# Kernel optimization log

Measured on AMD Instinct MI355X. Metric: run time of the kernel, lower is better.

The kernel has to match this reference:

```python
import jax, jax.numpy as jnp
import numpy as np

NP, P, H, NB = 14, 16, 12, 6  # n_patches per side, patch size, heads, blocks
HD, EMB, SEQ = 64, 768, NP * NP + 1


def _layernorm(x, g, b, eps=1e-5):
    m = x.mean(axis=-1, keepdims=True)
    v = x.var(axis=-1, keepdims=True)
    return (x - m) * jax.lax.rsqrt(v + eps) * g + b


def setup_inputs() -> dict:
    key = jax.random.key(0)
    ks = jax.random.split(key, 16)
    s = 0.02
    B = 64
    inp = {
        "images": jax.random.normal(ks[0], (B, 3, 224, 224), jnp.float32),
        "Wmap": jax.random.normal(ks[1], (768, 768), jnp.float32) * s,
        "bmap": jnp.zeros((768,), jnp.float32),
        "cls_tok": jax.random.normal(ks[2], (1, 768), jnp.float32) * s,
        "pos": jax.random.normal(ks[3], (SEQ, 768), jnp.float32) * s,
        "ln1_g": jnp.ones((NB, 768), jnp.float32),
        "ln1_b": jnp.zeros((NB, 768), jnp.float32),
        "Wq": jax.random.normal(ks[4], (NB, H, HD, HD), jnp.float32) * s,
        "bq": jnp.zeros((NB, H, HD), jnp.float32),
        "Wk": jax.random.normal(ks[5], (NB, H, HD, HD), jnp.float32) * s,
        "bk": jnp.zeros((NB, H, HD), jnp.float32),
        "Wv": jax.random.normal(ks[6], (NB, H, HD, HD), jnp.float32) * s,
        "bv": jnp.zeros((NB, H, HD), jnp.float32),
        "ln2_g": jnp.ones((NB, 768), jnp.float32),
        "ln2_b": jnp.zeros((NB, 768), jnp.float32),
        "W1": jax.random.normal(ks[7], (NB, 768, 3072), jnp.float32) * s,
        "b1": jnp.zeros((NB, 3072), jnp.float32),
        "W2": jax.random.normal(ks[8], (NB, 3072, 768), jnp.float32) * s,
        "b2": jnp.zeros((NB, 768), jnp.float32),
        "Whead": jax.random.normal(ks[9], (768, 10), jnp.float32) * s,
        "bhead": jnp.zeros((10,), jnp.float32),
    }
    return inp


def reference(images, Wmap, bmap, cls_tok, pos, ln1_g, ln1_b, Wq, bq, Wk, bk,
              Wv, bv, ln2_g, ln2_b, W1, b1, W2, b2, Whead, bhead):
    B = images.shape[0]
    # patchify: (B,3,224,224) -> (B,196,768); per-patch channel-first flatten
    x = images.reshape(B, 3, NP, P, NP, P)
    x = x.transpose(0, 2, 4, 1, 3, 5).reshape(B, NP * NP, 3 * P * P)
    tokens = x @ Wmap + bmap  # (B,196,768)
    tokens = jnp.concatenate(
        [jnp.broadcast_to(cls_tok[None], (B, 1, EMB)), tokens], axis=1)
    out = tokens + pos[None]  # (B,197,768)
    scale = 1.0 / jnp.sqrt(jnp.asarray(H, out.dtype))  # NOTE: source divides by sqrt(num_heads)
    for i in range(NB):
        h = _layernorm(out, ln1_g[i], ln1_b[i])
        xh = h.reshape(B, SEQ, H, HD)
        q = jnp.einsum('bshd,hde->bshe', xh, Wq[i]) + bq[i]
        k = jnp.einsum('bshd,hde->bshe', xh, Wk[i]) + bk[i]
        v = jnp.einsum('bshd,hde->bshe', xh, Wv[i]) + bv[i]
        attn = jax.nn.softmax(
            jnp.einsum('bqhd,bkhd->bhqk', q, k) * scale, axis=-1)
        o = jnp.einsum('bhqk,bkhd->bqhd', attn, v).reshape(B, SEQ, EMB)
        out = out + o
        h2 = _layernorm(out, ln2_g[i], ln2_b[i])
        mlp = jax.nn.gelu(h2 @ W1[i] + b1[i], approximate=False) @ W2[i] + b2[i]
        out = out + mlp
    cls = out[:, 0]  # (B,768)
    return jax.nn.softmax(cls @ Whead + bhead, axis=-1)
```

## Files before the change

kernel.cpp:

```cpp
#include <hip/hip_runtime.h>
#include <cstddef>

#define BATCH 64
#define SEQL  197
#define EMB   768
#define NH    12
#define HDIM  64
#define NBLK  6
#define MLPD  3072
#define TOKS  12608
#define PTOK  12544
#define ATT_SCALE 0.28867513459481287f
#define LOG2E 1.4426950408889634f

typedef short bf16x8 __attribute__((ext_vector_type(8)));
typedef float f32x4  __attribute__((ext_vector_type(4)));

__device__ inline float bf2f(unsigned short u) {
  union { unsigned int i; float f; } c; c.i = ((unsigned int)u) << 16; return c.f;
}
__device__ inline unsigned short f2bf(float f) {
  union { float f; unsigned int i; } c; c.f = f;
  unsigned int r = c.i + 0x7FFFu + ((c.i >> 16) & 1u);
  return (unsigned short)(r >> 16);
}

__device__ __forceinline__ void gload16(const unsigned short* g, void* l) {
  __builtin_amdgcn_global_load_lds(
      (const __attribute__((address_space(1))) unsigned int*)g,
      (__attribute__((address_space(3))) unsigned int*)l, 16, 0, 0);
}

__global__ __launch_bounds__(256) void patchify_kernel(const float* __restrict__ img,
                                                       unsigned short* __restrict__ out) {
  int i4 = blockIdx.x * 256 + threadIdx.x;
  int f4 = i4 % 192;
  int r  = i4 / 192;
  int b  = r / 196, t = r - b * 196;
  int f  = f4 * 4;
  int c  = f >> 8;
  int rem = f & 255;
  int iy = rem >> 4, ix = rem & 15;
  int py = t / 14, px = t - py * 14;
  const float* src = img + ((((size_t)b * 3 + c) * 224 + py * 16 + iy) * 224 + px * 16 + ix);
  float4 v = *(const float4*)src;
  ushort4 u;
  u.x = f2bf(v.x); u.y = f2bf(v.y); u.z = f2bf(v.z); u.w = f2bf(v.w);
  *(ushort4*)(out + (size_t)r * 768 + f) = u;
}

__global__ __launch_bounds__(256) void clspos_kernel(const float* __restrict__ cls,
                                                     const float* __restrict__ pos,
                                                     float* __restrict__ X) {
  int idx = blockIdx.x * 256 + threadIdx.x;
  int b = idx / 768, e = idx - b * 768;
  X[(size_t)b * SEQL * 768 + e] = cls[e] + pos[e];
}

__global__ __launch_bounds__(256) void wconv_kernel(const float* __restrict__ W,
                                                    unsigned short* __restrict__ Wt,
                                                    int K, int N) {
  __shared__ float t[32][33];
  int k0 = blockIdx.x * 32, n0 = blockIdx.y * 32;
  int kk = threadIdx.x >> 3, nn = (threadIdx.x & 7) * 4;
  float4 v = *(const float4*)&W[(size_t)(k0 + kk) * N + n0 + nn];
  t[nn + 0][kk] = v.x; t[nn + 1][kk] = v.y; t[nn + 2][kk] = v.z; t[nn + 3][kk] = v.w;
  __syncthreads();
  int nr = threadIdx.x >> 3, kc = (threadIdx.x & 7) * 4;
  ushort4 u;
  u.x = f2bf(t[nr][kc + 0]); u.y = f2bf(t[nr][kc + 1]);
  u.z = f2bf(t[nr][kc + 2]); u.w = f2bf(t[nr][kc + 3]);
  *(ushort4*)&Wt[(size_t)(n0 + nr) * K + k0 + kc] = u;
}

__global__ __launch_bounds__(256) void qwconv_kernel(const float* __restrict__ Wq,
                                                     const float* __restrict__ Wk,
                                                     const float* __restrict__ Wv,
                                                     unsigned short* __restrict__ Wt) {
  int mh = blockIdx.x;
  int m = mh / 12, h = mh - m * 12;
  const float* src = (m == 0 ? Wq : (m == 1 ? Wk : Wv)) + (size_t)h * 4096;
  unsigned short* dst = Wt + (size_t)mh * 4096;
  for (int idx = threadIdx.x; idx < 4096; idx += 256) {
    int d = idx >> 6, e = idx & 63;
    dst[e * 64 + d] = f2bf(src[idx]);
  }
}

template<int MODE>
__global__ __launch_bounds__(256, 2) void gemm_mfma(const unsigned short* __restrict__ A, int lda,
                                                    const unsigned short* __restrict__ Bt, int ldb,
                                                    void* __restrict__ Cv,
                                                    const float* __restrict__ bias,
                                                    const float* __restrict__ pos,
                                                    int M, int N, int K) {
  __shared__ short As[2][8192];
  __shared__ short Bs[2][8192];
  const int tid  = threadIdx.x;
  const int wid  = tid >> 6, lane = tid & 63;
  const int wr   = wid >> 1, wc = wid & 1;
  const int fr   = lane & 15;
  const int fq   = lane >> 4;
  const int m0   = blockIdx.y * 128;
  const int n0   = blockIdx.x * 128;
  const int srow = lane >> 3;
  const int schk = lane & 7;
  const int Mc   = M - 1;
  const int T    = K >> 6;

  f32x4 acc[4][4];
#pragma unroll
  for (int m = 0; m < 4; ++m)
#pragma unroll
    for (int n = 0; n < 4; ++n) acc[m][n] = (f32x4)0.f;

  auto STAGE = [&](int bufi, int k0) {
#pragma unroll
    for (int i = 0; i < 4; ++i) {
      int row = i * 32 + wid * 8 + srow;
      int gr = m0 + row; if (gr > Mc) gr = Mc;
      gload16(A + (size_t)gr * lda + k0 + ((schk ^ (row & 7)) << 3),
              (char*)&As[bufi][0] + i * 4096 + wid * 1024);
      gload16(Bt + (size_t)(n0 + row) * ldb + k0 + ((schk ^ (row & 7)) << 3),
              (char*)&Bs[bufi][0] + i * 4096 + wid * 1024);
    }
  };

  STAGE(0, 0);
  for (int t = 0; t < T; ++t) {
    const int c = t & 1;
    if (t + 1 < T) {
      STAGE(c ^ 1, (t + 1) << 6);
      asm volatile("s_waitcnt vmcnt(8)" ::: "memory");
    } else {
      asm volatile("s_waitcnt vmcnt(0)" ::: "memory");
    }
    __builtin_amdgcn_s_barrier();
    __builtin_amdgcn_sched_barrier(0);
#pragma unroll
    for (int ks = 0; ks < 2; ++ks) {
      bf16x8 af[4], bfr[4];
#pragma unroll
      for (int m = 0; m < 4; ++m) {
        int row = (wr << 6) + (m << 4) + fr;
        int ch = ((ks << 2) + fq) ^ (row & 7);
        af[m] = *(const bf16x8*)&As[c][(row << 6) + (ch << 3)];
      }
#pragma unroll
      for (int n = 0; n < 4; ++n) {
        int row = (wc << 6) + (n << 4) + fr;
        int ch = ((ks << 2) + fq) ^ (row & 7);
        bfr[n] = *(const bf16x8*)&Bs[c][(row << 6) + (ch << 3)];
      }
#pragma unroll
      for (int m = 0; m < 4; ++m)
#pragma unroll
        for (int n = 0; n < 4; ++n)
          acc[m][n] = __builtin_amdgcn_mfma_f32_16x16x32_bf16(af[m], bfr[n], acc[m][n], 0, 0, 0);
    }
    __builtin_amdgcn_sched_barrier(0);
    __builtin_amdgcn_s_barrier();
  }

#pragma unroll
  for (int m = 0; m < 4; ++m) {
#pragma unroll
    for (int j = 0; j < 4; ++j) {
      int r = m0 + (wr << 6) + (m << 4) + (fq << 2) + j;
      if (r >= M) continue;
#pragma unroll
      for (int n = 0; n < 4; ++n) {
        int c = n0 + (wc << 6) + (n << 4) + fr;
        float v = acc[m][n][j] + bias[c];
        if (MODE == 0) {
          int b = r / 196, t = r - b * 196;
          ((float*)Cv)[((size_t)b * SEQL + 1 + t) * 768 + c] = v + pos[(size_t)(1 + t) * 768 + c];
        } else if (MODE == 1) {
          float g = 0.5f * v * (1.f + erff(v * 0.70710678118654752f));
          ((unsigned short*)Cv)[(size_t)r * MLPD + c] = f2bf(g);
        } else {
          ((float*)Cv)[(size_t)r * 768 + c] += v;
        }
      }
    }
  }
}

__global__ __launch_bounds__(256) void ln_kernel(const float* __restrict__ Xi,
                                                 unsigned short* __restrict__ Ho,
                                                 const float* __restrict__ g,
                                                 const float* __restrict__ bb) {
  int tok = blockIdx.x * 4 + (threadIdx.x >> 6);
  int lane = threadIdx.x & 63;
  const float* x = Xi + (size_t)tok * 768;
  float4 v0 = *(const float4*)(x + lane * 4);
  float4 v1 = *(const float4*)(x + 256 + lane * 4);
  float4 v2 = *(const float4*)(x + 512 + lane * 4);
  float s = v0.x + v0.y + v0.z + v0.w + v1.x + v1.y + v1.z + v1.w + v2.x + v2.y + v2.z + v2.w;
  float q = v0.x*v0.x + v0.y*v0.y + v0.z*v0.z + v0.w*v0.w
          + v1.x*v1.x + v1.y*v1.y + v1.z*v1.z + v1.w*v1.w
          + v2.x*v2.x + v2.y*v2.y + v2.z*v2.z + v2.w*v2.w;
#pragma unroll
  for (int o = 32; o > 0; o >>= 1) { s += __shfl_xor(s, o); q += __shfl_xor(q, o); }
  float mean = s * (1.f / 768.f);
  float var  = q * (1.f / 768.f) - mean * mean;
  float rs = rsqrtf(var + 1e-5f);
  unsigned short* outp = Ho + (size_t)tok * 768;
  float4 g0 = *(const float4*)(g + lane * 4);
  float4 g1 = *(const float4*)(g + 256 + lane * 4);
  float4 g2 = *(const float4*)(g + 512 + lane * 4);
  float4 b0 = *(const float4*)(bb + lane * 4);
  float4 b1 = *(const float4*)(bb + 256 + lane * 4);
  float4 b2 = *(const float4*)(bb + 512 + lane * 4);
  ushort4 s0, s1, s2;
  s0.x = f2bf((v0.x - mean) * rs * g0.x + b0.x); s0.y = f2bf((v0.y - mean) * rs * g0.y + b0.y);
  s0.z = f2bf((v0.z - mean) * rs * g0.z + b0.z); s0.w = f2bf((v0.w - mean) * rs * g0.w + b0.w);
  s1.x = f2bf((v1.x - mean) * rs * g1.x + b1.x); s1.y = f2bf((v1.y - mean) * rs * g1.y + b1.y);
  s1.z = f2bf((v1.z - mean) * rs * g1.z + b1.z); s1.w = f2bf((v1.w - mean) * rs * g1.w + b1.w);
  s2.x = f2bf((v2.x - mean) * rs * g2.x + b2.x); s2.y = f2bf((v2.y - mean) * rs * g2.y + b2.y);
  s2.z = f2bf((v2.z - mean) * rs * g2.z + b2.z); s2.w = f2bf((v2.w - mean) * rs * g2.w + b2.w);
  *(ushort4*)(outp + lane * 4) = s0;
  *(ushort4*)(outp + 256 + lane * 4) = s1;
  *(ushort4*)(outp + 512 + lane * 4) = s2;
}

__global__ __launch_bounds__(256) void qkv_mfma(const unsigned short* __restrict__ Hb,
    const unsigned short* __restrict__ Wt,
    const float* __restrict__ bq, const float* __restrict__ bk, const float* __restrict__ bv,
    unsigned short* __restrict__ Qo, unsigned short* __restrict__ Ko,
    unsigned short* __restrict__ Vo) {
  const int h = blockIdx.y;
  const int tid = threadIdx.x, wv = tid >> 6, lane = tid & 63;
  const int fr = lane & 15, hi = lane >> 4;
  const int t0 = blockIdx.x * 64 + wv * 16;
  const unsigned short* arow = Hb + (size_t)(t0 + fr) * 768 + h * 64;
  bf16x8 a0 = *(const bf16x8*)(arow + hi * 8);
  bf16x8 a1 = *(const bf16x8*)(arow + 32 + hi * 8);
  f32x4 acc[3][4];
#pragma unroll
  for (int m = 0; m < 3; ++m)
#pragma unroll
    for (int n = 0; n < 4; ++n) acc[m][n] = (f32x4)0.f;
#pragma unroll
  for (int m = 0; m < 3; ++m) {
    const unsigned short* wb = Wt + (size_t)(m * 12 + h) * 4096;
#pragma unroll
    for (int n = 0; n < 4; ++n) {
      bf16x8 b0 = *(const bf16x8*)&wb[(n * 16 + fr) * 64 + hi * 8];
      bf16x8 b1 = *(const bf16x8*)&wb[(n * 16 + fr) * 64 + 32 + hi * 8];
      acc[m][n] = __builtin_amdgcn_mfma_f32_16x16x32_bf16(a0, b0, acc[m][n], 0, 0, 0);
      acc[m][n] = __builtin_amdgcn_mfma_f32_16x16x32_bf16(a1, b1, acc[m][n], 0, 0, 0);
    }
  }
#pragma unroll
  for (int m = 0; m < 3; ++m) {
    const float* bptr = (m == 0 ? bq : (m == 1 ? bk : bv)) + h * 64;
    unsigned short* optr = (m == 0 ? Qo : (m == 1 ? Ko : Vo));
    const float sc = (m == 0) ? ATT_SCALE : 1.f;
#pragma unroll
    for (int j = 0; j < 4; ++j) {
      int tk = t0 + hi * 4 + j;
      int b = tk / 197, s = tk - b * 197;
      size_t base_o = (((size_t)b * NH + h) * SEQL + s) * 64;
#pragma unroll
      for (int n = 0; n < 4; ++n)
        optr[base_o + n * 16 + fr] = f2bf((acc[m][n][j] + bptr[n * 16 + fr]) * sc);
    }
  }
}

__global__ __launch_bounds__(256) void attn_kernel(const unsigned short* __restrict__ Q,
                                                   const unsigned short* __restrict__ Kg,
                                                   const unsigned short* __restrict__ Vg,
                                                   float* __restrict__ X) {
  __shared__ unsigned short Vt[64][232];
  __shared__ unsigned short Pl[4][16][232];
  const int bh = blockIdx.x;
  const int b = bh / NH, h = bh - b * NH;
  const int tid = threadIdx.x, wv = tid >> 6, lane = tid & 63;
  const int fr = lane & 15, hi = lane >> 4;
  const unsigned short* Qp = Q  + (size_t)bh * SEQL * 64;
  const unsigned short* Kp = Kg + (size_t)bh * SEQL * 64;
  const unsigned short* Vp = Vg + (size_t)bh * SEQL * 64;

  for (int idx = tid; idx < SEQL * 16; idx += 256) {
    int s = idx >> 4, d4 = (idx & 15) * 4;
    ushort4 v = *(const ushort4*)&Vp[s * 64 + d4];
    Vt[d4 + 0][s] = v.x; Vt[d4 + 1][s] = v.y; Vt[d4 + 2][s] = v.z; Vt[d4 + 3][s] = v.w;
  }
  for (int idx = tid; idx < 64 * 35; idx += 256) {
    int d = idx / 35, c = 197 + idx % 35;
    Vt[d][c] = 0;
  }
  for (int idx = lane; idx < 16 * 24; idx += 64) {
    int r = idx / 24, c = 208 + idx % 24;
    Pl[wv][r][c] = 0;
  }
  __syncthreads();

  for (int qt = wv; qt < 13; qt += 4) {
    int qrow = qt * 16 + fr; if (qrow > 196) qrow = 196;
    bf16x8 qa0 = *(const bf16x8*)&Qp[qrow * 64 + hi * 8];
    bf16x8 qa1 = *(const bf16x8*)&Qp[qrow * 64 + 32 + hi * 8];
    f32x4 sc[13];
#pragma unroll
    for (int kt = 0; kt < 13; ++kt) {
      int krow = kt * 16 + fr; if (krow > 196) krow = 196;
      bf16x8 kb0 = *(const bf16x8*)&Kp[krow * 64 + hi * 8];
      bf16x8 kb1 = *(const bf16x8*)&Kp[krow * 64 + 32 + hi * 8];
      f32x4 a = (f32x4)0.f;
      a = __builtin_amdgcn_mfma_f32_16x16x32_bf16(qa0, kb0, a, 0, 0, 0);
      a = __builtin_amdgcn_mfma_f32_16x16x32_bf16(qa1, kb1, a, 0, 0, 0);
      sc[kt] = a;
    }
    float mx[4] = {-3e38f, -3e38f, -3e38f, -3e38f};
#pragma unroll
    for (int kt = 0; kt < 13; ++kt) {
      bool inval = (kt == 12) && (fr >= 5);
#pragma unroll
      for (int j = 0; j < 4; ++j) {
        float s = inval ? -3e38f : sc[kt][j];
        sc[kt][j] = s;
        mx[j] = fmaxf(mx[j], s);
      }
    }
#pragma unroll
    for (int o = 8; o > 0; o >>= 1)
#pragma unroll
      for (int j = 0; j < 4; ++j) mx[j] = fmaxf(mx[j], __shfl_xor(mx[j], o));
    float l[4] = {0.f, 0.f, 0.f, 0.f};
#pragma unroll
    for (int kt = 0; kt < 13; ++kt) {
#pragma unroll
      for (int j = 0; j < 4; ++j) {
        float p = exp2f((sc[kt][j] - mx[j]) * LOG2E);
        if ((kt == 12) && (fr >= 5)) p = 0.f;
        l[j] += p;
        Pl[wv][hi * 4 + j][kt * 16 + fr] = f2bf(p);
      }
    }
#pragma unroll
    for (int o = 8; o > 0; o >>= 1)
#pragma unroll
      for (int j = 0; j < 4; ++j) l[j] += __shfl_xor(l[j], o);
    f32x4 ov[4];
#pragma unroll
    for (int n = 0; n < 4; ++n) ov[n] = (f32x4)0.f;
#pragma unroll
    for (int kc = 0; kc < 7; ++kc) {
      bf16x8 pa = *(const bf16x8*)&Pl[wv][fr][kc * 32 + hi * 8];
#pragma unroll
      for (int n = 0; n < 4; ++n) {
        bf16x8 vb = *(const bf16x8*)&Vt[n * 16 + fr][kc * 32 + hi * 8];
        ov[n] = __builtin_amdgcn_mfma_f32_16x16x32_bf16(pa, vb, ov[n], 0, 0, 0);
      }
    }
#pragma unroll
    for (int j = 0; j < 4; ++j) {
      int r = qt * 16 + hi * 4 + j;
      if (r >= SEQL) continue;
      float inv = 1.f / l[j];
      float* xp = X + ((size_t)b * SEQL + r) * 768 + h * 64 + fr;
#pragma unroll
      for (int n = 0; n < 4; ++n) xp[n * 16] += ov[n][j] * inv;
    }
  }
}

__global__ __launch_bounds__(64) void head_kernel(const float* __restrict__ X,
                                                  const float* __restrict__ Wh,
                                                  const float* __restrict__ bh,
                                                  float* __restrict__ out) {
  __shared__ float lg[10];
  int b = blockIdx.x, t = threadIdx.x;
  if (t < 10) {
    float acc = bh[t];
    const float* x = X + (size_t)b * SEQL * 768;
    for (int d = 0; d < 768; ++d) acc += x[d] * Wh[d * 10 + t];
    lg[t] = acc;
  }
  __syncthreads();
  if (t == 0) {
    float m = lg[0];
    for (int c = 1; c < 10; ++c) m = fmaxf(m, lg[c]);
    float ssum = 0.f;
    for (int c = 0; c < 10; ++c) ssum += expf(lg[c] - m);
    for (int c = 0; c < 10; ++c) out[b * 10 + c] = expf(lg[c] - m) / ssum;
  }
}

extern "C" void kernel_launch(void* const* d_in, const int* in_sizes, int n_in,
                              void* d_out, int out_size, void* d_ws, size_t ws_size,
                              hipStream_t stream) {
  const float* images = (const float*)d_in[0];
  const float* Wmap = (const float*)d_in[1];
  const float* bmap = (const float*)d_in[2];
  const float* cls  = (const float*)d_in[3];
  const float* pos  = (const float*)d_in[4];
  const float* ln1g = (const float*)d_in[5];
  const float* ln1b = (const float*)d_in[6];
  const float* Wq   = (const float*)d_in[7];
  const float* bq   = (const float*)d_in[8];
  const float* Wk   = (const float*)d_in[9];
  const float* bk   = (const float*)d_in[10];
  const float* Wv   = (const float*)d_in[11];
  const float* bv   = (const float*)d_in[12];
  const float* ln2g = (const float*)d_in[13];
  const float* ln2b = (const float*)d_in[14];
  const float* W1   = (const float*)d_in[15];
  const float* b1   = (const float*)d_in[16];
  const float* W2   = (const float*)d_in[17];
  const float* b2   = (const float*)d_in[18];
  const float* Wh   = (const float*)d_in[19];
  const float* bhd  = (const float*)d_in[20];
  float* out = (float*)d_out;

  const size_t ACT = (size_t)TOKS * 768;
  const size_t oX = 0;
  const size_t oHb = oX + ACT * 4;
  const size_t oR  = oHb + ACT * 2;
  const size_t oW1 = oR + 3 * ACT * 4;
  const size_t oW2 = oW1 + (size_t)768 * 3072 * 2;
  const size_t oWm = oW2 + (size_t)768 * 3072 * 2;
  const size_t oQW = oWm + (size_t)768 * 768 * 2;
  const size_t need = oQW + (size_t)36 * 4096 * 2;
  if (ws_size < need) return;

  char* ws = (char*)d_ws;
  float* X = (float*)(ws + oX);
  unsigned short* Hb = (unsigned short*)(ws + oHb);
  unsigned short* Qb = (unsigned short*)(ws + oR);
  unsigned short* Kb = Qb + ACT;
  unsigned short* Vb = Kb + ACT;
  unsigned short* mid = (unsigned short*)(ws + oR);
  unsigned short* patches = (unsigned short*)(ws + oR);
  unsigned short* W1t = (unsigned short*)(ws + oW1);
  unsigned short* W2t = (unsigned short*)(ws + oW2);
  unsigned short* Wmapt = (unsigned short*)(ws + oWm);
  unsigned short* QWt = (unsigned short*)(ws + oQW);

  wconv_kernel<<<dim3(24, 24), 256, 0, stream>>>(Wmap, Wmapt, 768, 768);
  patchify_kernel<<<9408, 256, 0, stream>>>(images, patches);
  clspos_kernel<<<192, 256, 0, stream>>>(cls, pos, X);
  gemm_mfma<0><<<dim3(6, 98), 256, 0, stream>>>(patches, 768, Wmapt, 768, X, bmap, pos,
                                                PTOK, 768, 768);

  for (int i = 0; i < NBLK; ++i) {
    ln_kernel<<<3152, 256, 0, stream>>>(X, Hb, ln1g + i * 768, ln1b + i * 768);
    qwconv_kernel<<<36, 256, 0, stream>>>(Wq + (size_t)i * 49152, Wk + (size_t)i * 49152,
                                          Wv + (size_t)i * 49152, QWt);
    qkv_mfma<<<dim3(197, 12), 256, 0, stream>>>(Hb, QWt,
        bq + i * 768, bk + i * 768, bv + i * 768, Qb, Kb, Vb);
    attn_kernel<<<768, 256, 0, stream>>>(Qb, Kb, Vb, X);
    ln_kernel<<<3152, 256, 0, stream>>>(X, Hb, ln2g + i * 768, ln2b + i * 768);
    wconv_kernel<<<dim3(24, 96), 256, 0, stream>>>(W1 + (size_t)i * 2359296, W1t, 768, MLPD);
    wconv_kernel<<<dim3(96, 24), 256, 0, stream>>>(W2 + (size_t)i * 2359296, W2t, MLPD, 768);
    gemm_mfma<1><<<dim3(24, 99), 256, 0, stream>>>(Hb, 768, W1t, 768, mid, b1 + i * MLPD,
                                                   nullptr, TOKS, MLPD, 768);
    gemm_mfma<2><<<dim3(6, 99), 256, 0, stream>>>(mid, MLPD, W2t, MLPD, X, b2 + i * 768,
                                                  nullptr, TOKS, 768, MLPD);
  }
  head_kernel<<<64, 64, 0, stream>>>(X, Wh, bhd, out);
}
```

Before: 2.360 ms.

## Replace 128x128 GEMM with 256x256 tiles, XCD-aware block remap, interleaved staging

Replaces the 128x128-tile, 4-wave GEMM with a 256x256-tile, 8-wave kernel that keeps 8x4 MFMA accumulators per wave. Tile coordinates now come from a 1D grid remapped per XCD so neighbouring tiles share L2. Global loads for the next k-step are split and interleaved with MFMA phases, with raised wave priority around the MFMA bursts. The goal is more operand reuse per LDS byte and better overlap of loads with compute. The cost is 128KB of LDS and higher register pressure per block, and fewer blocks overall, which can leave CUs idle at the tail (e.g. 150 blocks for the W2 GEMM and 147 for patch embedding).

```diff
diff --git a/kernel.cpp b/kernel.cpp
--- a/kernel.cpp
+++ b/kernel.cpp
@@ -88,93 +88,104 @@
 }
 
 template<int MODE>
-__global__ __launch_bounds__(256, 2) void gemm_mfma(const unsigned short* __restrict__ A, int lda,
-                                                    const unsigned short* __restrict__ Bt, int ldb,
-                                                    void* __restrict__ Cv,
-                                                    const float* __restrict__ bias,
-                                                    const float* __restrict__ pos,
-                                                    int M, int N, int K) {
-  __shared__ short As[2][8192];
-  __shared__ short Bs[2][8192];
+__global__ __launch_bounds__(512, 2) void gemm256(const unsigned short* __restrict__ A, int lda,
+                                                  const unsigned short* __restrict__ Bt, int ldb,
+                                                  void* __restrict__ Cv,
+                                                  const float* __restrict__ bias,
+                                                  const float* __restrict__ pos,
+                                                  int M, int K, int GX) {
+  __shared__ short As[2][16384];
+  __shared__ short Bs[2][16384];
+  const int nwg = gridDim.x;
+  const int orig = blockIdx.x;
+  const int qq = nwg >> 3, rr = nwg & 7, xcd = orig & 7, idx = orig >> 3;
+  const int wg = (xcd < rr ? xcd * (qq + 1) : rr * (qq + 1) + (xcd - rr) * qq) + idx;
+  const int m0 = (wg / GX) * 256;
+  const int n0 = (wg % GX) * 256;
+
   const int tid  = threadIdx.x;
   const int wid  = tid >> 6, lane = tid & 63;
-  const int wr   = wid >> 1, wc = wid & 1;
+  const int wr   = wid >> 2, wc = wid & 3;
   const int fr   = lane & 15;
   const int fq   = lane >> 4;
-  const int m0   = blockIdx.y * 128;
-  const int n0   = blockIdx.x * 128;
+  const int frk  = fr & 7;
   const int srow = lane >> 3;
   const int schk = lane & 7;
   const int Mc   = M - 1;
   const int T    = K >> 6;
 
-  f32x4 acc[4][4];
-#pragma unroll
-  for (int m = 0; m < 4; ++m)
+  f32x4 acc[8][4];
+#pragma unroll
+  for (int m = 0; m < 8; ++m)
 #pragma unroll
     for (int n = 0; n < 4; ++n) acc[m][n] = (f32x4)0.f;
 
-  auto STAGE = [&](int bufi, int k0) {
-#pragma unroll
-    for (int i = 0; i < 4; ++i) {
-      int row = i * 32 + wid * 8 + srow;
-      int gr = m0 + row; if (gr > Mc) gr = Mc;
-      gload16(A + (size_t)gr * lda + k0 + ((schk ^ (row & 7)) << 3),
-              (char*)&As[bufi][0] + i * 4096 + wid * 1024);
-      gload16(Bt + (size_t)(n0 + row) * ldb + k0 + ((schk ^ (row & 7)) << 3),
-              (char*)&Bs[bufi][0] + i * 4096 + wid * 1024);
-    }
+  auto STAGE_PART = [&](int bufi, int k0, int p) {
+    int row = p * 64 + wid * 8 + srow;
+    int gra = m0 + row; if (gra > Mc) gra = Mc;
+    gload16(A + (size_t)gra * lda + k0 + ((schk ^ srow) << 3),
+            (char*)&As[bufi][0] + p * 8192 + wid * 1024);
+    int grb = n0 + row;
+    gload16(Bt + (size_t)grb * ldb + k0 + ((schk ^ srow) << 3),
+            (char*)&Bs[bufi][0] + p * 8192 + wid * 1024);
   };
 
-  STAGE(0, 0);
+#pragma unroll
+  for (int p = 0; p < 4; ++p) STAGE_PART(0, 0, p);
+#pragma unroll
+  for (int p = 0; p < 4; ++p) STAGE_PART(1, 64, p);
+  asm volatile("s_waitcnt vmcnt(8)" ::: "memory");
+  __builtin_amdgcn_s_barrier();
+
   for (int t = 0; t < T; ++t) {
-    const int c = t & 1;
-    if (t + 1 < T) {
-      STAGE(c ^ 1, (t + 1) << 6);
-      asm volatile("s_waitcnt vmcnt(8)" ::: "memory");
-    } else {
-      asm volatile("s_waitcnt vmcnt(0)" ::: "memory");
-    }
-    __builtin_amdgcn_s_barrier();
-    __builtin_amdgcn_sched_barrier(0);
-#pragma unroll
-    for (int ks = 0; ks < 2; ++ks) {
-      bf16x8 af[4], bfr[4];
-#pragma unroll
-      for (int m = 0; m < 4; ++m) {
-        int row = (wr << 6) + (m << 4) + fr;
-        int ch = ((ks << 2) + fq) ^ (row & 7);
-        af[m] = *(const bf16x8*)&As[c][(row << 6) + (ch << 3)];
+    const int b = t & 1;
+    const short* Ab = &As[b][wr * 8192];
+    const short* Bb = &Bs[b][(wc >> 1) * 8192 + (wc & 1) * 4096];
+    const bool st = (t >= 1) && (t + 1 < T);
+    const int nk = (t + 1) << 6;
+#pragma unroll
+    for (int p = 0; p < 4; ++p) {
+      if (st) {
+        if (p == 0) { STAGE_PART(b ^ 1, nk, 0); STAGE_PART(b ^ 1, nk, 1); }
+        if (p == 1) { STAGE_PART(b ^ 1, nk, 2); STAGE_PART(b ^ 1, nk, 3); }
       }
+      const int mg = p >> 1, ks = p & 1;
+      const int slot = ((ks << 2) + fq) ^ frk;
+      bf16x8 af[4], bfv[4];
+#pragma unroll
+      for (int mi = 0; mi < 4; ++mi)
+        af[mi] = *(const bf16x8*)&Ab[((mg * 4 + mi) * 16 + fr) * 64 + slot * 8];
+#pragma unroll
+      for (int n = 0; n < 4; ++n)
+        bfv[n] = *(const bf16x8*)&Bb[(n * 16 + fr) * 64 + slot * 8];
+      __builtin_amdgcn_sched_barrier(0);
+      __builtin_amdgcn_s_setprio(1);
+#pragma unroll
+      for (int mi = 0; mi < 4; ++mi)
+#pragma unroll
+        for (int n = 0; n < 4; ++n)
+          acc[mg * 4 + mi][n] =
+              __builtin_amdgcn_mfma_f32_16x16x32_bf16(af[mi], bfv[n], acc[mg * 4 + mi][n], 0, 0, 0);
+      __builtin_amdgcn_s_setprio(0);
+      __builtin_amdgcn_sched_barrier(0);
+      if (p == 3) asm volatile("s_waitcnt vmcnt(0)" ::: "memory");
+      __builtin_amdgcn_s_barrier();
+    }
+  }
+
+#pragma unroll
+  for (int m = 0; m < 8; ++m) {
+#pragma unroll
+    for (int j = 0; j < 4; ++j) {
+      int r = m0 + wr * 128 + m * 16 + (fq << 2) + j;
+      if (r >= M) continue;
 #pragma unroll
       for (int n = 0; n < 4; ++n) {
-        int row = (wc << 6) + (n << 4) + fr;
-        int ch = ((ks << 2) + fq) ^ (row & 7);
-        bfr[n] = *(const bf16x8*)&Bs[c][(row << 6) + (ch << 3)];
-      }
-#pragma unroll
-      for (int m = 0; m < 4; ++m)
-#pragma unroll
-        for (int n = 0; n < 4; ++n)
-          acc[m][n] = __builtin_amdgcn_mfma_f32_16x16x32_bf16(af[m], bfr[n], acc[m][n], 0, 0, 0);
-    }
-    __builtin_amdgcn_sched_barrier(0);
-    __builtin_amdgcn_s_barrier();
-  }
-
-#pragma unroll
-  for (int m = 0; m < 4; ++m) {
-#pragma unroll
-    for (int j = 0; j < 4; ++j) {
-      int r = m0 + (wr << 6) + (m << 4) + (fq << 2) + j;
-      if (r >= M) continue;
-#pragma unroll
-      for (int n = 0; n < 4; ++n) {
-        int c = n0 + (wc << 6) + (n << 4) + fr;
+        int c = n0 + wc * 64 + n * 16 + fr;
         float v = acc[m][n][j] + bias[c];
         if (MODE == 0) {
-          int b = r / 196, t = r - b * 196;
-          ((float*)Cv)[((size_t)b * SEQL + 1 + t) * 768 + c] = v + pos[(size_t)(1 + t) * 768 + c];
+          int bb = r / 196, tt = r - bb * 196;
+          ((float*)Cv)[((size_t)bb * SEQL + 1 + tt) * 768 + c] = v + pos[(size_t)(1 + tt) * 768 + c];
         } else if (MODE == 1) {
           float g = 0.5f * v * (1.f + erff(v * 0.70710678118654752f));
           ((unsigned short*)Cv)[(size_t)r * MLPD + c] = f2bf(g);
@@ -442,8 +453,8 @@
   wconv_kernel<<<dim3(24, 24), 256, 0, stream>>>(Wmap, Wmapt, 768, 768);
   patchify_kernel<<<9408, 256, 0, stream>>>(images, patches);
   clspos_kernel<<<192, 256, 0, stream>>>(cls, pos, X);
-  gemm_mfma<0><<<dim3(6, 98), 256, 0, stream>>>(patches, 768, Wmapt, 768, X, bmap, pos,
-                                                PTOK, 768, 768);
+  gemm256<0><<<147, 512, 0, stream>>>(patches, 768, Wmapt, 768, X, bmap, pos,
+                                      PTOK, 768, 3);
 
   for (int i = 0; i < NBLK; ++i) {
     ln_kernel<<<3152, 256, 0, stream>>>(X, Hb, ln1g + i * 768, ln1b + i * 768);
@@ -455,10 +466,10 @@
     ln_kernel<<<3152, 256, 0, stream>>>(X, Hb, ln2g + i * 768, ln2b + i * 768);
     wconv_kernel<<<dim3(24, 96), 256, 0, stream>>>(W1 + (size_t)i * 2359296, W1t, 768, MLPD);
     wconv_kernel<<<dim3(96, 24), 256, 0, stream>>>(W2 + (size_t)i * 2359296, W2t, MLPD, 768);
-    gemm_mfma<1><<<dim3(24, 99), 256, 0, stream>>>(Hb, 768, W1t, 768, mid, b1 + i * MLPD,
-                                                   nullptr, TOKS, MLPD, 768);
-    gemm_mfma<2><<<dim3(6, 99), 256, 0, stream>>>(mid, MLPD, W2t, MLPD, X, b2 + i * 768,
-                                                  nullptr, TOKS, 768, MLPD);
+    gemm256<1><<<600, 512, 0, stream>>>(Hb, 768, W1t, 768, mid, b1 + i * MLPD,
+                                        nullptr, TOKS, 768, 12);
+    gemm256<2><<<150, 512, 0, stream>>>(mid, MLPD, W2t, MLPD, X, b2 + i * 768,
+                                        nullptr, TOKS, 3072, 3);
   }
   head_kernel<<<64, 64, 0, stream>>>(X, Wh, bhd, out);
 }
```

Result: slower. 2.586 ms (+9.6%).

## Add 256x256-tile double-buffered GEMM with XCD-aware remap for MLP up-projection

Applied to the files above, without the earlier changes.

Adds a new gemm256 kernel that uses 256x256 output tiles, 512 threads, double-buffered LDS and a workgroup-to-XCD remapping, and uses it for the W1 GELU GEMM. The larger tile raises operand reuse per LDS load, and the remap groups neighbouring tiles on the same XCD to share L2. Separately, the old gemm_mfma, still used for patch embedding and W2, loses its double buffering and now syncs with plain __syncthreads. That likely slows those GEMMs by exposing global load latency.

```diff
diff --git a/kernel.cpp b/kernel.cpp
--- a/kernel.cpp
+++ b/kernel.cpp
@@ -88,14 +88,14 @@
 }
 
 template<int MODE>
-__global__ __launch_bounds__(256, 2) void gemm_mfma(const unsigned short* __restrict__ A, int lda,
-                                                    const unsigned short* __restrict__ Bt, int ldb,
-                                                    void* __restrict__ Cv,
-                                                    const float* __restrict__ bias,
-                                                    const float* __restrict__ pos,
-                                                    int M, int N, int K) {
-  __shared__ short As[2][8192];
-  __shared__ short Bs[2][8192];
+__global__ __launch_bounds__(256) void gemm_mfma(const unsigned short* __restrict__ A, int lda,
+                                                 const unsigned short* __restrict__ Bt, int ldb,
+                                                 void* __restrict__ Cv,
+                                                 const float* __restrict__ bias,
+                                                 const float* __restrict__ pos,
+                                                 int M, int N, int K) {
+  __shared__ short As[8192];
+  __shared__ short Bs[8192];
   const int tid  = threadIdx.x;
   const int wid  = tid >> 6, lane = tid & 63;
   const int wr   = wid >> 1, wc = wid & 1;
@@ -106,7 +106,6 @@
   const int srow = lane >> 3;
   const int schk = lane & 7;
   const int Mc   = M - 1;
-  const int T    = K >> 6;
 
   f32x4 acc[4][4];
 #pragma unroll
@@ -114,29 +113,17 @@
 #pragma unroll
     for (int n = 0; n < 4; ++n) acc[m][n] = (f32x4)0.f;
 
-  auto STAGE = [&](int bufi, int k0) {
+  for (int k0 = 0; k0 < K; k0 += 64) {
 #pragma unroll
     for (int i = 0; i < 4; ++i) {
       int row = i * 32 + wid * 8 + srow;
       int gr = m0 + row; if (gr > Mc) gr = Mc;
       gload16(A + (size_t)gr * lda + k0 + ((schk ^ (row & 7)) << 3),
-              (char*)&As[bufi][0] + i * 4096 + wid * 1024);
+              (char*)As + i * 4096 + wid * 1024);
       gload16(Bt + (size_t)(n0 + row) * ldb + k0 + ((schk ^ (row & 7)) << 3),
-              (char*)&Bs[bufi][0] + i * 4096 + wid * 1024);
-    }
-  };
-
-  STAGE(0, 0);
-  for (int t = 0; t < T; ++t) {
-    const int c = t & 1;
-    if (t + 1 < T) {
-      STAGE(c ^ 1, (t + 1) << 6);
-      asm volatile("s_waitcnt vmcnt(8)" ::: "memory");
-    } else {
-      asm volatile("s_waitcnt vmcnt(0)" ::: "memory");
-    }
-    __builtin_amdgcn_s_barrier();
-    __builtin_amdgcn_sched_barrier(0);
+              (char*)Bs + i * 4096 + wid * 1024);
+    }
+    __syncthreads();
 #pragma unroll
     for (int ks = 0; ks < 2; ++ks) {
       bf16x8 af[4], bfr[4];
@@ -144,13 +131,13 @@
       for (int m = 0; m < 4; ++m) {
         int row = (wr << 6) + (m << 4) + fr;
         int ch = ((ks << 2) + fq) ^ (row & 7);
-        af[m] = *(const bf16x8*)&As[c][(row << 6) + (ch << 3)];
+        af[m] = *(const bf16x8*)&As[(row << 6) + (ch << 3)];
       }
 #pragma unroll
       for (int n = 0; n < 4; ++n) {
         int row = (wc << 6) + (n << 4) + fr;
         int ch = ((ks << 2) + fq) ^ (row & 7);
-        bfr[n] = *(const bf16x8*)&Bs[c][(row << 6) + (ch << 3)];
+        bfr[n] = *(const bf16x8*)&Bs[(row << 6) + (ch << 3)];
       }
 #pragma unroll
       for (int m = 0; m < 4; ++m)
@@ -158,8 +145,7 @@
         for (int n = 0; n < 4; ++n)
           acc[m][n] = __builtin_amdgcn_mfma_f32_16x16x32_bf16(af[m], bfr[n], acc[m][n], 0, 0, 0);
     }
-    __builtin_amdgcn_sched_barrier(0);
-    __builtin_amdgcn_s_barrier();
+    __syncthreads();
   }
 
 #pragma unroll
@@ -176,6 +162,108 @@
           int b = r / 196, t = r - b * 196;
           ((float*)Cv)[((size_t)b * SEQL + 1 + t) * 768 + c] = v + pos[(size_t)(1 + t) * 768 + c];
         } else if (MODE == 1) {
+          float g = 0.5f * v * (1.f + erff(v * 0.70710678118654752f));
+          ((unsigned short*)Cv)[(size_t)r * MLPD + c] = f2bf(g);
+        } else {
+          ((float*)Cv)[(size_t)r * 768 + c] += v;
+        }
+      }
+    }
+  }
+}
+
+template<int MODE>
+__global__ __launch_bounds__(512, 2) void gemm256(const unsigned short* __restrict__ A, int lda,
+                                                  const unsigned short* __restrict__ Bt, int ldb,
+                                                  void* __restrict__ Cv,
+                                                  const float* __restrict__ bias,
+                                                  int M, int K, int GX) {
+  __shared__ short As[2][16384];
+  __shared__ short Bs[2][16384];
+  const int nwg = gridDim.x;
+  const int orig = blockIdx.x;
+  const int qq = nwg >> 3, rr = nwg & 7, xcd = orig & 7, bidx = orig >> 3;
+  const int wg = (xcd < rr ? xcd * (qq + 1) : rr * (qq + 1) + (xcd - rr) * qq) + bidx;
+  const int m0 = (wg / GX) * 256;
+  const int n0 = (wg % GX) * 256;
+
+  const int tid  = threadIdx.x;
+  const int wid  = tid >> 6, lane = tid & 63;
+  const int wr   = wid >> 2, wc = wid & 3;
+  const int fr   = lane & 15;
+  const int fq   = lane >> 4;
+  const int frk  = fr & 7;
+  const int srow = lane >> 3;
+  const int schk = lane & 7;
+  const int Mc   = M - 1;
+  const int T    = K >> 6;
+
+  f32x4 acc[8][4];
+#pragma unroll
+  for (int m = 0; m < 8; ++m)
+#pragma unroll
+    for (int n = 0; n < 4; ++n) acc[m][n] = (f32x4)0.f;
+
+  auto STAGE = [&](int bufi, int k0) {
+#pragma unroll
+    for (int p = 0; p < 4; ++p) {
+      int row = p * 64 + wid * 8 + srow;
+      int gra = m0 + row; if (gra > Mc) gra = Mc;
+      gload16(A + (size_t)gra * lda + k0 + ((schk ^ srow) << 3),
+              (char*)&As[bufi][0] + p * 8192 + wid * 1024);
+      int grb = n0 + row;
+      gload16(Bt + (size_t)grb * ldb + k0 + ((schk ^ srow) << 3),
+              (char*)&Bs[bufi][0] + p * 8192 + wid * 1024);
+    }
+  };
+
+  STAGE(0, 0);
+  for (int t = 0; t < T; ++t) {
+    const int b = t & 1;
+    if (t + 1 < T) {
+      STAGE(b ^ 1, (t + 1) << 6);
+      asm volatile("s_waitcnt vmcnt(8)" ::: "memory");
+    } else {
+      asm volatile("s_waitcnt vmcnt(0)" ::: "memory");
+    }
+    __builtin_amdgcn_s_barrier();
+    const short* Ab = &As[b][wr * 8192];
+    const short* Bb = &Bs[b][wc * 4096];
+#pragma unroll
+    for (int mg = 0; mg < 2; ++mg) {
+#pragma unroll
+      for (int ks = 0; ks < 2; ++ks) {
+        const int slot = ((ks << 2) + fq) ^ frk;
+        bf16x8 af[4], bfv[4];
+#pragma unroll
+        for (int mi = 0; mi < 4; ++mi)
+          af[mi] = *(const bf16x8*)&Ab[((mg * 4 + mi) * 16 + fr) * 64 + slot * 8];
+#pragma unroll
+        for (int n = 0; n < 4; ++n)
+          bfv[n] = *(const bf16x8*)&Bb[(n * 16 + fr) * 64 + slot * 8];
+#pragma unroll
+        for (int mi = 0; mi < 4; ++mi)
+#pragma unroll
+          for (int n = 0; n < 4; ++n)
+            acc[mg * 4 + mi][n] =
+                __builtin_amdgcn_mfma_f32_16x16x32_bf16(af[mi], bfv[n], acc[mg * 4 + mi][n], 0, 0, 0);
+      }
+    }
+    __builtin_amdgcn_sched_barrier(0);
+    __builtin_amdgcn_s_barrier();
+  }
+
+#pragma unroll
+  for (int m = 0; m < 8; ++m) {
+#pragma unroll
+    for (int j = 0; j < 4; ++j) {
+      int r = m0 + wr * 128 + m * 16 + (fq << 2) + j;
+      if (r >= M) continue;
+#pragma unroll
+      for (int n = 0; n < 4; ++n) {
+        int c = n0 + wc * 64 + n * 16 + fr;
+        float v = acc[m][n][j] + bias[c];
+        if (MODE == 1) {
           float g = 0.5f * v * (1.f + erff(v * 0.70710678118654752f));
           ((unsigned short*)Cv)[(size_t)r * MLPD + c] = f2bf(g);
         } else {
@@ -455,8 +543,8 @@
     ln_kernel<<<3152, 256, 0, stream>>>(X, Hb, ln2g + i * 768, ln2b + i * 768);
     wconv_kernel<<<dim3(24, 96), 256, 0, stream>>>(W1 + (size_t)i * 2359296, W1t, 768, MLPD);
     wconv_kernel<<<dim3(96, 24), 256, 0, stream>>>(W2 + (size_t)i * 2359296, W2t, MLPD, 768);
-    gemm_mfma<1><<<dim3(24, 99), 256, 0, stream>>>(Hb, 768, W1t, 768, mid, b1 + i * MLPD,
-                                                   nullptr, TOKS, MLPD, 768);
+    gemm256<1><<<600, 512, 0, stream>>>(Hb, 768, W1t, 768, mid, b1 + i * MLPD,
+                                        TOKS, 768, 12);
     gemm_mfma<2><<<dim3(6, 99), 256, 0, stream>>>(mid, MLPD, W2t, MLPD, X, b2 + i * 768,
                                                   nullptr, TOKS, 768, MLPD);
   }
```

Result: no change. 2.321 ms (-1.7%).
